# Kernel optimization log

Measured on AMD Instinct MI355X. Metric: run time of the kernel, lower is better.

## Reference

```python
import jax, jax.numpy as jnp
import numpy as np

NUM_BOND_TYPE = 6
NUM_BOND_DIRECTION = 3
N_NODES = 20000
N_EDGES = 320000
HIDDEN = 256
OUT = 256
N_MASK = 2000


def setup_inputs() -> dict:
    key = jax.random.key(0)
    ks = jax.random.split(key, 12)
    x = jax.random.normal(ks[0], (N_NODES, HIDDEN), dtype=jnp.float32)
    edge_index = jax.random.randint(ks[1], (2, N_EDGES), 0, N_NODES, dtype=jnp.int64)
    edge_attr = jax.random.randint(ks[2], (N_EDGES, 2), 0, 3, dtype=jnp.int64)
    mask_node_indices = jax.random.randint(ks[3], (N_MASK,), 0, N_NODES, dtype=jnp.int64)
    # parameters (torch Linear convention: y = x @ W.T + b)
    def xavier(k, shape):
        fan_in, fan_out = shape[1], shape[0]
        lim = float(np.sqrt(6.0 / (fan_in + fan_out)))
        return jax.random.uniform(k, shape, jnp.float32, -lim, lim)
    prelu_a = jnp.asarray(0.25, dtype=jnp.float32)  # torch PReLU default
    W_enc = xavier(ks[4], (HIDDEN, HIDDEN))          # enc_to_dec, no bias
    E1 = xavier(ks[5], (NUM_BOND_TYPE, HIDDEN))
    E2 = xavier(ks[6], (NUM_BOND_DIRECTION, HIDDEN))
    W1 = xavier(ks[7], (2 * HIDDEN, HIDDEN))
    b1 = jnp.zeros((2 * HIDDEN,), jnp.float32)
    W2 = xavier(ks[8], (OUT, 2 * HIDDEN))
    b2 = jnp.zeros((OUT,), jnp.float32)
    return {"x": x, "edge_index": edge_index, "edge_attr": edge_attr,
            "mask_node_indices": mask_node_indices, "prelu_a": prelu_a,
            "W_enc": W_enc, "E1": E1, "E2": E2,
            "W1": W1, "b1": b1, "W2": W2, "b2": b2}


def reference(x, edge_index, edge_attr, mask_node_indices, prelu_a,
              W_enc, E1, E2, W1, b1, W2, b2):
    N = x.shape[0]
    # PReLU -> enc_to_dec linear (no bias) -> zero masked rows
    x = jnp.where(x >= 0, x, prelu_a * x)
    x = x @ W_enc.T
    x = x.at[mask_node_indices].set(0.0)
    # add self loops: (i,i) edges with attr (4, 0)
    loop = jnp.arange(N, dtype=edge_index.dtype)
    ei = jnp.concatenate([edge_index, jnp.stack([loop, loop])], axis=1)  # [2, E+N]
    loop_attr = jnp.concatenate(
        [jnp.full((N, 1), 4, edge_attr.dtype), jnp.zeros((N, 1), edge_attr.dtype)], axis=1)
    ea = jnp.concatenate([edge_attr, loop_attr], axis=0)                 # [E+N, 2]
    edge_emb = E1[ea[:, 0]] + E2[ea[:, 1]]                               # [E+N, D]
    src, dst = ei[0], ei[1]                                              # j -> i
    msg = x[src] + edge_emb                                              # [E+N, D]
    aggr = jax.ops.segment_sum(msg, dst, num_segments=N)                 # [N, D]
    # GIN MLP: Linear -> ReLU -> Linear
    h = jax.nn.relu(aggr @ W1.T + b1)
    return h @ W2.T + b2
```

## Files before the change

kernel.cpp:

```cpp
#include <hip/hip_runtime.h>

#define HIDDEN 256
#define CAP 64

typedef _Float16 h4_t __attribute__((ext_vector_type(4)));
typedef _Float16 h8_t __attribute__((ext_vector_type(8)));
typedef float    f4_t __attribute__((ext_vector_type(4)));

typedef const __attribute__((address_space(1))) void* gbl_ptr_t;
typedef __attribute__((address_space(3))) void*       lds_ptr_t;

template<int N> struct IC { static constexpr int v = N; };
template<int...> struct Seq {};
template<int N, int... Is> struct MkSeq : MkSeq<N - 1, N - 1, Is...> {};
template<int... Is> struct MkSeq<0, Is...> { using t = Seq<Is...>; };
template<typename F, int... Is>
__device__ __forceinline__ void unroll_for(F&& f, Seq<Is...>) { (f(IC<Is>{}), ...); }

template<int N> __device__ __forceinline__ void vmwait() {
    asm volatile("s_waitcnt vmcnt(%0)" :: "n"(N) : "memory");
}

__device__ inline f4_t cvt4(h4_t h) {
    f4_t o; o.x = (float)h.x; o.y = (float)h.y; o.z = (float)h.z; o.w = (float)h.w;
    return o;
}

__global__ __launch_bounds__(256) void k_prep(
        const float* __restrict__ x, _Float16* __restrict__ xh,
        const float* __restrict__ prelu_a, int M, int Mpad, int nb_x,
        const int* __restrict__ ei, const int* __restrict__ ea, int E,
        int* __restrict__ cnt, int* __restrict__ csr, int nb_fill,
        const float* __restrict__ W_enc, const float* __restrict__ W1,
        const float* __restrict__ W2, _Float16* __restrict__ Whenc,
        _Float16* __restrict__ Wh1, _Float16* __restrict__ Wh2, int nb_w,
        const int* __restrict__ mask, unsigned char* __restrict__ flags, int NM) {
    int b = blockIdx.x;
    int t = threadIdx.x;
    if (b < nb_x) {
        int base = (b * 256 + t) * 4;
        if (base >= Mpad * HIDDEN) return;
        int row = base >> 8;
        h4_t o;
        if (row < M) {
            float pa = *prelu_a;
            f4_t v = *(const f4_t*)(x + base);
            o.x = (_Float16)(v.x >= 0.f ? v.x : pa * v.x);
            o.y = (_Float16)(v.y >= 0.f ? v.y : pa * v.y);
            o.z = (_Float16)(v.z >= 0.f ? v.z : pa * v.z);
            o.w = (_Float16)(v.w >= 0.f ? v.w : pa * v.w);
        } else {
            o = (h4_t)(_Float16)0.f;
        }
        *(h4_t*)(xh + base) = o;
        return;
    }
    b -= nb_x;
    if (b < nb_fill) {
        int e = b * 256 + t;
        if (e >= E) return;
        int src = ei[e];
        int dst = ei[E + e];
        int combo = ea[2 * e] * 3 + ea[2 * e + 1];
        int slot = atomicAdd(&cnt[dst], 1);
        if (slot < CAP) csr[dst * CAP + slot] = src | (combo << 16);
        return;
    }
    b -= nb_fill;
    if (b < nb_w) {
        const int n0 = HIDDEN * HIDDEN, n1 = 2 * HIDDEN * HIDDEN, n2 = HIDDEN * 2 * HIDDEN;
        int base = (b * 256 + t) * 4;
        const float* s; _Float16* d; int off;
        if (base < n0) { s = W_enc; d = Whenc; off = base; }
        else if (base < n0 + n1) { s = W1; d = Wh1; off = base - n0; }
        else if (base < n0 + n1 + n2) { s = W2; d = Wh2; off = base - n0 - n1; }
        else return;
        f4_t v = *(const f4_t*)(s + off);
        h4_t o; o.x = (_Float16)v.x; o.y = (_Float16)v.y;
        o.z = (_Float16)v.z; o.w = (_Float16)v.w;
        *(h4_t*)(d + off) = o;
        return;
    }
    b -= nb_w;
    {
        int i = b * 256 + t;
        if (i < NM) flags[mask[i]] = 1;
    }
}

__global__ __launch_bounds__(256) void k_aggregate(
        const _Float16* __restrict__ xe,
        const float* __restrict__ E1, const float* __restrict__ E2,
        const int* __restrict__ cnt, const int* __restrict__ csr,
        _Float16* __restrict__ aggr, int N, int Mpad) {
    __shared__ __align__(16) _Float16 e12h[18 * HIDDEN];
    int t = threadIdx.x;
    for (int idx = t; idx < 18 * 64; idx += 256) {
        int combo = idx >> 6, c4 = (idx & 63) * 4;
        int a1 = combo / 3, a2 = combo - a1 * 3;
        f4_t v1 = *(const f4_t*)(E1 + a1 * HIDDEN + c4);
        f4_t v2 = *(const f4_t*)(E2 + a2 * HIDDEN + c4);
        h4_t o;
        o.x = (_Float16)(v1.x + v2.x); o.y = (_Float16)(v1.y + v2.y);
        o.z = (_Float16)(v1.z + v2.z); o.w = (_Float16)(v1.w + v2.w);
        *(h4_t*)(e12h + combo * HIDDEN + c4) = o;
    }
    __syncthreads();
    int node = blockIdx.x * 4 + (t >> 6);
    if (node >= Mpad) return;
    int lane = t & 63;
    int c0 = lane * 4;
    if (node >= N) {
        *(h4_t*)(aggr + (size_t)node * HIDDEN + c0) = (h4_t)(_Float16)0.f;
        return;
    }
    int deg = cnt[node];
    if (deg > CAP) deg = CAP;
    const int* lst = csr + (size_t)node * CAP;
    int pv = (lane < deg) ? lst[lane] : 0;

    h4_t hs = *(const h4_t*)(xe + (size_t)node * HIDDEN + c0);
    h4_t se = *(const h4_t*)(e12h + 12 * HIDDEN + c0);
    f4_t acc = cvt4(hs) + cvt4(se);

    int e = 0;
    for (; e + 7 < deg; e += 8) {
        int p[8]; h4_t hv[8], qv[8];
#pragma unroll
        for (int j = 0; j < 8; ++j) p[j] = __shfl(pv, e + j, 64);
#pragma unroll
        for (int j = 0; j < 8; ++j)
            hv[j] = *(const h4_t*)(xe + (size_t)(p[j] & 0xFFFF) * HIDDEN + c0);
#pragma unroll
        for (int j = 0; j < 8; ++j)
            qv[j] = *(const h4_t*)(e12h + (p[j] >> 16) * HIDDEN + c0);
        h4_t s0 = (hv[0] + qv[0]) + (hv[1] + qv[1]);
        h4_t s1 = (hv[2] + qv[2]) + (hv[3] + qv[3]);
        h4_t s2 = (hv[4] + qv[4]) + (hv[5] + qv[5]);
        h4_t s3 = (hv[6] + qv[6]) + (hv[7] + qv[7]);
        acc += cvt4(s0) + cvt4(s1);
        acc += cvt4(s2) + cvt4(s3);
    }
    for (; e < deg; ++e) {
        int p = __shfl(pv, e, 64);
        h4_t h = *(const h4_t*)(xe + (size_t)(p & 0xFFFF) * HIDDEN + c0);
        h4_t q = *(const h4_t*)(e12h + (p >> 16) * HIDDEN + c0);
        acc += cvt4(h + q);
    }
    h4_t o;
    o.x = (_Float16)acc.x; o.y = (_Float16)acc.y;
    o.z = (_Float16)acc.z; o.w = (_Float16)acc.w;
    *(h4_t*)(aggr + (size_t)node * HIDDEN + c0) = o;
}

template <int TM, int K, bool RELU, bool HAS_BIAS, bool OUT_F16, bool MASK>
__global__ __launch_bounds__(64) void k_gemm64(
        const _Float16* __restrict__ A, const _Float16* __restrict__ B,
        const float* __restrict__ bias, void* __restrict__ Cout,
        const unsigned char* __restrict__ flags, int Mstore, int N) {
    constexpr int BM  = TM * 16;
    constexpr int RB  = 4;
    constexpr int NS  = K / 32;
    constexpr int LPS = TM + 4;
    __shared__ __align__(16) _Float16 As[RB][BM * 32];
    __shared__ __align__(16) _Float16 Bs[RB][64 * 32];
    int L = threadIdx.x;
    int m0 = blockIdx.x * BM, n0 = blockIdx.y * 64;
    int lr = L & 15, lk = (L >> 4) * 8;

    f4_t acc[TM][4] = {};

    auto stage = [&](int s) {
        int k0 = s * 32, r = s & (RB - 1);
#pragma unroll
        for (int i = 0; i < TM; ++i) {
            int c = L + 64 * i;
            __builtin_amdgcn_global_load_lds(
                (gbl_ptr_t)(A + (size_t)(m0 + (c >> 2)) * K + k0 + (c & 3) * 8),
                (lds_ptr_t)(As[r] + c * 8), 16, 0, 0);
        }
#pragma unroll
        for (int i = 0; i < 4; ++i) {
            int c = L + 64 * i;
            __builtin_amdgcn_global_load_lds(
                (gbl_ptr_t)(B + (size_t)(n0 + (c >> 2)) * K + k0 + (c & 3) * 8),
                (lds_ptr_t)(Bs[r] + c * 8), 16, 0, 0);
        }
    };

    unroll_for([&](auto P) { stage(P.v); }, typename MkSeq<RB>::t{});

    unroll_for([&](auto SC) {
        constexpr int s = SC.v;
        constexpr int issued = (RB + s < NS) ? RB + s : NS;
        vmwait<(issued - s - 1) * LPS>();
        h8_t af[TM], bf[4];
        const _Float16* as = As[s & (RB - 1)];
        const _Float16* bs = Bs[s & (RB - 1)];
#pragma unroll
        for (int i = 0; i < TM; ++i) af[i] = *(const h8_t*)&as[(i * 16 + lr) * 32 + lk];
#pragma unroll
        for (int j = 0; j < 4; ++j)  bf[j] = *(const h8_t*)&bs[(j * 16 + lr) * 32 + lk];
        asm volatile("s_waitcnt lgkmcnt(0)" ::: "memory");
        if constexpr (s + RB < NS) stage(s + RB);
#pragma unroll
        for (int i = 0; i < TM; ++i)
#pragma unroll
            for (int j = 0; j < 4; ++j)
                acc[i][j] = __builtin_amdgcn_mfma_f32_16x16x32_f16(af[i], bf[j], acc[i][j], 0, 0, 0);
    }, typename MkSeq<NS>::t{});

    int lr4 = (L >> 4) * 4;
#pragma unroll
    for (int i = 0; i < TM; ++i)
#pragma unroll
        for (int r = 0; r < 4; ++r) {
            int row = m0 + i * 16 + lr4 + r;
            float zm = (MASK && flags[row]) ? 0.f : 1.f;
#pragma unroll
            for (int j = 0; j < 4; ++j) {
                int col = n0 + j * 16 + lr;
                float v = acc[i][j][r];
                if (HAS_BIAS) v += bias[col];
                if (RELU) v = v > 0.f ? v : 0.f;
                v *= zm;
                if (OUT_F16) {
                    ((_Float16*)Cout)[(size_t)row * N + col] = (_Float16)v;
                } else {
                    if (row < Mstore) ((float*)Cout)[(size_t)row * N + col] = v;
                }
            }
        }
}

extern "C" void kernel_launch(void* const* d_in, const int* in_sizes, int n_in,
                              void* d_out, int out_size, void* d_ws, size_t ws_size,
                              hipStream_t stream) {
    const float* x       = (const float*)d_in[0];
    const int*   ei      = (const int*)d_in[1];
    const int*   ea      = (const int*)d_in[2];
    const int*   mask    = (const int*)d_in[3];
    const float* prelu_a = (const float*)d_in[4];
    const float* W_enc   = (const float*)d_in[5];
    const float* E1      = (const float*)d_in[6];
    const float* E2      = (const float*)d_in[7];
    const float* W1      = (const float*)d_in[8];
    const float* b1      = (const float*)d_in[9];
    const float* W2      = (const float*)d_in[10];
    const float* b2      = (const float*)d_in[11];
    float*       out     = (float*)d_out;

    int N  = in_sizes[0] / HIDDEN;
    int E  = in_sizes[1] / 2;
    int NM = in_sizes[3];
    int Mpad = ((N + 127) / 128) * 128;

    char* ws = (char*)d_ws;
    size_t off = 0;
    _Float16* xh    = (_Float16*)(ws + off); off += (size_t)Mpad * HIDDEN * 2;
    _Float16* XEh   = (_Float16*)(ws + off); off += (size_t)Mpad * HIDDEN * 2;
    _Float16* AGh   = (_Float16*)(ws + off); off += (size_t)Mpad * HIDDEN * 2;
    _Float16* Hh    = (_Float16*)(ws + off); off += (size_t)Mpad * 2 * HIDDEN * 2;
    _Float16* Whenc = (_Float16*)(ws + off); off += (size_t)HIDDEN * HIDDEN * 2;
    _Float16* Wh1   = (_Float16*)(ws + off); off += (size_t)2 * HIDDEN * HIDDEN * 2;
    _Float16* Wh2   = (_Float16*)(ws + off); off += (size_t)HIDDEN * 2 * HIDDEN * 2;
    int* cnt        = (int*)(ws + off);      off += (size_t)N * 4;
    unsigned char* flags = (unsigned char*)(ws + off); off += (size_t)Mpad;
    off = (off + 15) & ~(size_t)15;
    int* csr        = (int*)(ws + off);      off += (size_t)N * CAP * 4;

    hipMemsetAsync(cnt, 0, (size_t)N * 4 + (size_t)Mpad, stream);

    int nb_x    = (Mpad * HIDDEN / 4 + 255) / 256;
    int nb_fill = (E + 255) / 256;
    int wtot4   = (HIDDEN * HIDDEN + 2 * HIDDEN * HIDDEN + HIDDEN * 2 * HIDDEN) / 4;
    int nb_w    = (wtot4 + 255) / 256;
    int nb_m    = (NM + 255) / 256;
    k_prep<<<nb_x + nb_fill + nb_w + nb_m, 256, 0, stream>>>(
        x, xh, prelu_a, N, Mpad, nb_x,
        ei, ea, E, cnt, csr, nb_fill,
        W_enc, W1, W2, Whenc, Wh1, Wh2, nb_w,
        mask, flags, NM);

    dim3 g1(Mpad / 64, HIDDEN / 64);
    k_gemm64<4, HIDDEN, false, false, true, true><<<g1, 64, 0, stream>>>(
        xh, Whenc, nullptr, XEh, flags, N, HIDDEN);

    k_aggregate<<<(Mpad + 3) / 4, 256, 0, stream>>>(XEh, E1, E2, cnt, csr, AGh, N, Mpad);

    dim3 g2(Mpad / 64, 2 * HIDDEN / 64);
    k_gemm64<4, HIDDEN, true, true, true, false><<<g2, 64, 0, stream>>>(
        AGh, Wh1, b1, Hh, nullptr, N, 2 * HIDDEN);

    dim3 g3(Mpad / 64, HIDDEN / 64);
    k_gemm64<4, 2 * HIDDEN, false, true, false, false><<<g3, 64, 0, stream>>>(
        Hh, Wh2, b2, out, nullptr, N, HIDDEN);
}
```

Baseline: 207.6 us.

## Fuse PReLU into first GEMM and load GEMM operands directly to registers

Removes the separate PReLU/fp16 conversion pass over x: the first GEMM now reads fp32 x directly, applies PReLU and converts to fp16 in registers. All three GEMMs switch from a single-wave LDS-staged multi-buffer pipeline to a 4-wave block where each wave loads its A and B fragments straight from global memory into registers, double-buffered. This saves one full read and write of the activation matrix and the LDS round trip. In exchange, B tiles are no longer shared through LDS, so each wave re-fetches weights and per-wave tiles shrink to 32 rows.

```diff
diff --git a/kernel.cpp b/kernel.cpp
--- a/kernel.cpp
+++ b/kernel.cpp
@@ -6,9 +6,6 @@
 typedef _Float16 h4_t __attribute__((ext_vector_type(4)));
 typedef _Float16 h8_t __attribute__((ext_vector_type(8)));
 typedef float    f4_t __attribute__((ext_vector_type(4)));
-
-typedef const __attribute__((address_space(1))) void* gbl_ptr_t;
-typedef __attribute__((address_space(3))) void*       lds_ptr_t;
 
 template<int N> struct IC { static constexpr int v = N; };
 template<int...> struct Seq {};
@@ -17,18 +14,12 @@
 template<typename F, int... Is>
 __device__ __forceinline__ void unroll_for(F&& f, Seq<Is...>) { (f(IC<Is>{}), ...); }
 
-template<int N> __device__ __forceinline__ void vmwait() {
-    asm volatile("s_waitcnt vmcnt(%0)" :: "n"(N) : "memory");
-}
-
 __device__ inline f4_t cvt4(h4_t h) {
     f4_t o; o.x = (float)h.x; o.y = (float)h.y; o.z = (float)h.z; o.w = (float)h.w;
     return o;
 }
 
 __global__ __launch_bounds__(256) void k_prep(
-        const float* __restrict__ x, _Float16* __restrict__ xh,
-        const float* __restrict__ prelu_a, int M, int Mpad, int nb_x,
         const int* __restrict__ ei, const int* __restrict__ ea, int E,
         int* __restrict__ cnt, int* __restrict__ csr, int nb_fill,
         const float* __restrict__ W_enc, const float* __restrict__ W1,
@@ -37,25 +28,6 @@
         const int* __restrict__ mask, unsigned char* __restrict__ flags, int NM) {
     int b = blockIdx.x;
     int t = threadIdx.x;
-    if (b < nb_x) {
-        int base = (b * 256 + t) * 4;
-        if (base >= Mpad * HIDDEN) return;
-        int row = base >> 8;
-        h4_t o;
-        if (row < M) {
-            float pa = *prelu_a;
-            f4_t v = *(const f4_t*)(x + base);
-            o.x = (_Float16)(v.x >= 0.f ? v.x : pa * v.x);
-            o.y = (_Float16)(v.y >= 0.f ? v.y : pa * v.y);
-            o.z = (_Float16)(v.z >= 0.f ? v.z : pa * v.z);
-            o.w = (_Float16)(v.w >= 0.f ? v.w : pa * v.w);
-        } else {
-            o = (h4_t)(_Float16)0.f;
-        }
-        *(h4_t*)(xh + base) = o;
-        return;
-    }
-    b -= nb_x;
     if (b < nb_fill) {
         int e = b * 256 + t;
         if (e >= E) return;
@@ -153,61 +125,81 @@
     *(h4_t*)(aggr + (size_t)node * HIDDEN + c0) = o;
 }
 
-template <int TM, int K, bool RELU, bool HAS_BIAS, bool OUT_F16, bool MASK>
-__global__ __launch_bounds__(64) void k_gemm64(
-        const _Float16* __restrict__ A, const _Float16* __restrict__ B,
+template <int TM, int K, bool RELU, bool HAS_BIAS, bool OUT_F16, bool MASK, bool A_F32>
+__global__ __launch_bounds__(256) void k_gemm_reg(
+        const void* __restrict__ Ain, const _Float16* __restrict__ B,
         const float* __restrict__ bias, void* __restrict__ Cout,
-        const unsigned char* __restrict__ flags, int Mstore, int N) {
-    constexpr int BM  = TM * 16;
-    constexpr int RB  = 4;
-    constexpr int NS  = K / 32;
-    constexpr int LPS = TM + 4;
-    __shared__ __align__(16) _Float16 As[RB][BM * 32];
-    __shared__ __align__(16) _Float16 Bs[RB][64 * 32];
-    int L = threadIdx.x;
-    int m0 = blockIdx.x * BM, n0 = blockIdx.y * 64;
+        const unsigned char* __restrict__ flags, const float* __restrict__ prelu_a,
+        int Mload, int Mstore, int N) {
+    constexpr int BM = TM * 16;
+    constexpr int NS = K / 32;
+    int t = threadIdx.x;
+    int wv = t >> 6, L = t & 63;
+    int m0 = (blockIdx.x * 4 + wv) * BM;
+    int n0 = blockIdx.y * 64;
     int lr = L & 15, lk = (L >> 4) * 8;
 
+    const _Float16* Ah = (const _Float16*)Ain;
+    const float*    Af = (const float*)Ain;
+    float pa = 0.f;
+    if constexpr (A_F32) pa = *prelu_a;
+
     f4_t acc[TM][4] = {};
-
-    auto stage = [&](int s) {
-        int k0 = s * 32, r = s & (RB - 1);
+    h8_t fa[2][TM];
+    f4_t fa32[2][TM][2];
+    h8_t fb[2][4];
+
+    auto LOAD = [&](auto SC, auto BC) {
+        constexpr int s = SC.v, bb = BC.v;
+        const int k0 = s * 32;
 #pragma unroll
         for (int i = 0; i < TM; ++i) {
-            int c = L + 64 * i;
-            __builtin_amdgcn_global_load_lds(
-                (gbl_ptr_t)(A + (size_t)(m0 + (c >> 2)) * K + k0 + (c & 3) * 8),
-                (lds_ptr_t)(As[r] + c * 8), 16, 0, 0);
+            int row = m0 + i * 16 + lr;
+            if constexpr (A_F32) {
+                f4_t u = {0.f, 0.f, 0.f, 0.f}, v2 = {0.f, 0.f, 0.f, 0.f};
+                if (row < Mload) {
+                    const float* p = Af + (size_t)row * K + k0 + lk;
+                    u  = *(const f4_t*)p;
+                    v2 = *(const f4_t*)(p + 4);
+                }
+                fa32[bb][i][0] = u; fa32[bb][i][1] = v2;
+            } else {
+                fa[bb][i] = *(const h8_t*)(Ah + (size_t)row * K + k0 + lk);
+            }
         }
 #pragma unroll
-        for (int i = 0; i < 4; ++i) {
-            int c = L + 64 * i;
-            __builtin_amdgcn_global_load_lds(
-                (gbl_ptr_t)(B + (size_t)(n0 + (c >> 2)) * K + k0 + (c & 3) * 8),
-                (lds_ptr_t)(Bs[r] + c * 8), 16, 0, 0);
+        for (int j = 0; j < 4; ++j)
+            fb[bb][j] = *(const h8_t*)(B + (size_t)(n0 + j * 16 + lr) * K + k0 + lk);
+    };
+
+    LOAD(IC<0>{}, IC<0>{});
+    unroll_for([&](auto SC) {
+        constexpr int s = SC.v, bb = s & 1;
+        if constexpr (s + 1 < NS) LOAD(IC<s + 1>{}, IC<bb ^ 1>{});
+        h8_t af[TM];
+#pragma unroll
+        for (int i = 0; i < TM; ++i) {
+            if constexpr (A_F32) {
+                f4_t u = fa32[bb][i][0], v2 = fa32[bb][i][1];
+                h8_t o;
+                o[0] = (_Float16)(u.x  >= 0.f ? u.x  : pa * u.x);
+                o[1] = (_Float16)(u.y  >= 0.f ? u.y  : pa * u.y);
+                o[2] = (_Float16)(u.z  >= 0.f ? u.z  : pa * u.z);
+                o[3] = (_Float16)(u.w  >= 0.f ? u.w  : pa * u.w);
+                o[4] = (_Float16)(v2.x >= 0.f ? v2.x : pa * v2.x);
+                o[5] = (_Float16)(v2.y >= 0.f ? v2.y : pa * v2.y);
+                o[6] = (_Float16)(v2.z >= 0.f ? v2.z : pa * v2.z);
+                o[7] = (_Float16)(v2.w >= 0.f ? v2.w : pa * v2.w);
+                af[i] = o;
+            } else {
+                af[i] = fa[bb][i];
+            }
         }
-    };
-
-    unroll_for([&](auto P) { stage(P.v); }, typename MkSeq<RB>::t{});
-
-    unroll_for([&](auto SC) {
-        constexpr int s = SC.v;
-        constexpr int issued = (RB + s < NS) ? RB + s : NS;
-        vmwait<(issued - s - 1) * LPS>();
-        h8_t af[TM], bf[4];
-        const _Float16* as = As[s & (RB - 1)];
-        const _Float16* bs = Bs[s & (RB - 1)];
-#pragma unroll
-        for (int i = 0; i < TM; ++i) af[i] = *(const h8_t*)&as[(i * 16 + lr) * 32 + lk];
-#pragma unroll
-        for (int j = 0; j < 4; ++j)  bf[j] = *(const h8_t*)&bs[(j * 16 + lr) * 32 + lk];
-        asm volatile("s_waitcnt lgkmcnt(0)" ::: "memory");
-        if constexpr (s + RB < NS) stage(s + RB);
 #pragma unroll
         for (int i = 0; i < TM; ++i)
 #pragma unroll
             for (int j = 0; j < 4; ++j)
-                acc[i][j] = __builtin_amdgcn_mfma_f32_16x16x32_f16(af[i], bf[j], acc[i][j], 0, 0, 0);
+                acc[i][j] = __builtin_amdgcn_mfma_f32_16x16x32_f16(af[i], fb[bb][j], acc[i][j], 0, 0, 0);
     }, typename MkSeq<NS>::t{});
 
     int lr4 = (L >> 4) * 4;
@@ -216,15 +208,16 @@
 #pragma unroll
         for (int r = 0; r < 4; ++r) {
             int row = m0 + i * 16 + lr4 + r;
-            float zm = (MASK && flags[row]) ? 0.f : 1.f;
+            float zm = 1.f;
+            if constexpr (MASK) zm = flags[row] ? 0.f : 1.f;
 #pragma unroll
             for (int j = 0; j < 4; ++j) {
                 int col = n0 + j * 16 + lr;
                 float v = acc[i][j][r];
-                if (HAS_BIAS) v += bias[col];
-                if (RELU) v = v > 0.f ? v : 0.f;
+                if constexpr (HAS_BIAS) v += bias[col];
+                if constexpr (RELU) v = v > 0.f ? v : 0.f;
                 v *= zm;
-                if (OUT_F16) {
+                if constexpr (OUT_F16) {
                     ((_Float16*)Cout)[(size_t)row * N + col] = (_Float16)v;
                 } else {
                     if (row < Mstore) ((float*)Cout)[(size_t)row * N + col] = v;
@@ -257,7 +250,6 @@
 
     char* ws = (char*)d_ws;
     size_t off = 0;
-    _Float16* xh    = (_Float16*)(ws + off); off += (size_t)Mpad * HIDDEN * 2;
     _Float16* XEh   = (_Float16*)(ws + off); off += (size_t)Mpad * HIDDEN * 2;
     _Float16* AGh   = (_Float16*)(ws + off); off += (size_t)Mpad * HIDDEN * 2;
     _Float16* Hh    = (_Float16*)(ws + off); off += (size_t)Mpad * 2 * HIDDEN * 2;
@@ -271,28 +263,26 @@
 
     hipMemsetAsync(cnt, 0, (size_t)N * 4 + (size_t)Mpad, stream);
 
-    int nb_x    = (Mpad * HIDDEN / 4 + 255) / 256;
     int nb_fill = (E + 255) / 256;
     int wtot4   = (HIDDEN * HIDDEN + 2 * HIDDEN * HIDDEN + HIDDEN * 2 * HIDDEN) / 4;
     int nb_w    = (wtot4 + 255) / 256;
     int nb_m    = (NM + 255) / 256;
-    k_prep<<<nb_x + nb_fill + nb_w + nb_m, 256, 0, stream>>>(
-        x, xh, prelu_a, N, Mpad, nb_x,
+    k_prep<<<nb_fill + nb_w + nb_m, 256, 0, stream>>>(
         ei, ea, E, cnt, csr, nb_fill,
         W_enc, W1, W2, Whenc, Wh1, Wh2, nb_w,
         mask, flags, NM);
 
-    dim3 g1(Mpad / 64, HIDDEN / 64);
-    k_gemm64<4, HIDDEN, false, false, true, true><<<g1, 64, 0, stream>>>(
-        xh, Whenc, nullptr, XEh, flags, N, HIDDEN);
+    dim3 g1(Mpad / 128, HIDDEN / 64);
+    k_gemm_reg<2, HIDDEN, false, false, true, true, true><<<g1, 256, 0, stream>>>(
+        x, Whenc, nullptr, XEh, flags, prelu_a, N, N, HIDDEN);
 
     k_aggregate<<<(Mpad + 3) / 4, 256, 0, stream>>>(XEh, E1, E2, cnt, csr, AGh, N, Mpad);
 
-    dim3 g2(Mpad / 64, 2 * HIDDEN / 64);
-    k_gemm64<4, HIDDEN, true, true, true, false><<<g2, 64, 0, stream>>>(
-        AGh, Wh1, b1, Hh, nullptr, N, 2 * HIDDEN);
-
-    dim3 g3(Mpad / 64, HIDDEN / 64);
-    k_gemm64<4, 2 * HIDDEN, false, true, false, false><<<g3, 64, 0, stream>>>(
-        Hh, Wh2, b2, out, nullptr, N, HIDDEN);
-}
+    dim3 g2(Mpad / 128, 2 * HIDDEN / 64);
+    k_gemm_reg<2, HIDDEN, true, true, true, false, false><<<g2, 256, 0, stream>>>(
+        AGh, Wh1, b1, Hh, nullptr, nullptr, Mpad, N, 2 * HIDDEN);
+
+    dim3 g3(Mpad / 128, HIDDEN / 64);
+    k_gemm_reg<2, 2 * HIDDEN, false, true, false, false, false><<<g3, 256, 0, stream>>>(
+        Hh, Wh2, b2, out, nullptr, nullptr, Mpad, N, HIDDEN);
+}
```

Result: slower. 226.6 us (+9.1%).
